# Kernel tuning notes

Hardware: AMD Instinct MI355X
Metric: run time of the kernel (lower is better)

The kernel has to match this reference:

```python
import jax, jax.numpy as jnp
import numpy as np

N, IN_DIM, D, H, M = 50000, 256, 256, 4, 3
C = D // H
E = 800000
EPS = 1e-5
NEG_SLOPE = 0.2


def setup_inputs() -> dict:
    key = jax.random.key(0)
    ks = jax.random.split(key, 16)
    inp = {
        'feat': jax.random.normal(ks[0], (N, IN_DIM), jnp.float32),
        'Wl': jax.random.normal(ks[1], (IN_DIM, D), jnp.float32) * (1.0 / np.sqrt(IN_DIM)),
        'bl': jnp.zeros((D,), jnp.float32),
        'Wr': jax.random.normal(ks[2], (IN_DIM, D), jnp.float32) * (1.0 / np.sqrt(IN_DIM)),
        'br': jnp.zeros((D,), jnp.float32),
        'attn_l': jax.random.normal(ks[3], (M, H, C), jnp.float32) * 0.1,
        'attn_r': jax.random.normal(ks[4], (M, H, C), jnp.float32) * 0.1,
        'rel_attn_l': jax.random.normal(ks[5], (H, C), jnp.float32) * 0.1,
        'rel_attn_r': jax.random.normal(ks[6], (H, C), jnp.float32) * 0.1,
        'ln_gamma': jnp.ones((D,), jnp.float32),
        'ln_beta': jnp.zeros((D,), jnp.float32),
    }
    for m in range(M):
        inp[f'src{m}'] = jax.random.randint(ks[7 + 2 * m], (E,), 0, N, jnp.int32)
        inp[f'dst{m}'] = jax.random.randint(ks[8 + 2 * m], (E,), 0, N, jnp.int32)
    return inp


def _latte_forward(feat, Wl, bl, Wr, br, attn_l, attn_r, rel_attn_l, rel_attn_r,
                   ln_gamma, ln_beta, edges):
    n = feat.shape[0]
    k = (feat @ Wl + bl).reshape(n, H, C)   # src projection
    v = (feat @ Wr + br).reshape(n, H, C)   # dst projection
    # per-node attention logit halves (equivalent to per-edge dot products)
    al = jnp.einsum('nhc,mhc->mnh', k, attn_l)  # [M,N,H]
    ar = jnp.einsum('nhc,mhc->mnh', v, attn_r)  # [M,N,H]
    hs = []
    for m, (src, dst) in enumerate(edges):
        att = al[m][src] + ar[m][dst]                  # [E,H]
        att = jax.nn.leaky_relu(att, NEG_SLOPE)        # attn_activation (dropout=identity, eval)
        # segment softmax over incoming edges of each dst node
        amax = jax.ops.segment_max(att, dst, num_segments=n)      # [N,H]
        ex = jnp.exp(att - amax[dst])                              # [E,H]
        denom = jax.ops.segment_sum(ex, dst, num_segments=n)      # [N,H]
        w = ex / denom[dst]                                        # softmax weights
        # message h = dst's v (faithful to edge_attention: {'h': edges.dst['v']})
        h = jax.ops.segment_sum(w[:, :, None] * v[dst], dst, num_segments=n)  # [N,H,C]
        hs.append(h)
    out = jnp.stack(hs + [v], axis=1)                  # [N,M+1,H,C]
    # relation-level beta attention; key = out[:, -1] = v
    alpha_l = jnp.einsum('nhc,hc->nh', v, rel_attn_l)          # [N,H]
    alpha_r = jnp.einsum('nrhc,hc->nrh', out, rel_attn_r)      # [N,M+1,H]
    beta = jax.nn.softmax(jax.nn.leaky_relu(alpha_l[:, None, :] + alpha_r, NEG_SLOPE), axis=2)
    o = (out * beta[..., None]).sum(axis=1).reshape(n, D)
    # LayerNorm
    mu = o.mean(axis=-1, keepdims=True)
    var = ((o - mu) ** 2).mean(axis=-1, keepdims=True)
    o = (o - mu) / jnp.sqrt(var + EPS) * ln_gamma + ln_beta
    return jax.nn.relu(o)  # dropout = identity in eval mode


def reference(feat, Wl, bl, Wr, br, attn_l, attn_r, rel_attn_l, rel_attn_r,
              ln_gamma, ln_beta, src0, dst0, src1, dst1, src2, dst2):
    edges = [(src0, dst0), (src1, dst1), (src2, dst2)]
    return _latte_forward(feat, Wl, bl, Wr, br, attn_l, attn_r,
                          rel_attn_l, rel_attn_r, ln_gamma, ln_beta, edges)
```

## Files before the change

kernel.cpp:

```cpp
#include <hip/hip_runtime.h>


#define NN 50000
#define NT 3125
#define NB 782
#define NEG 0.2f
#define EPSV 1e-5f

typedef __attribute__((ext_vector_type(8))) short bf16x8;
typedef __attribute__((ext_vector_type(4))) float f32x4;

#define LDS_FENCE() asm volatile("s_waitcnt lgkmcnt(0)" ::: "memory")

__device__ __forceinline__ short f2bf(float f) {
    unsigned u = __float_as_uint(f);
    u += 0x7fff + ((u >> 16) & 1);
    return (short)(u >> 16);
}

__device__ __forceinline__ void ld_g2l_16(void* lds, const void* g) {
    __builtin_amdgcn_global_load_lds(
        (const __attribute__((address_space(1))) unsigned int*)g,
        (__attribute__((address_space(3))) unsigned int*)lds, 16, 0, 0);
}
__device__ __forceinline__ void ld_g2l_4(void* lds, const void* g) {
    __builtin_amdgcn_global_load_lds(
        (const __attribute__((address_space(1))) unsigned int*)g,
        (__attribute__((address_space(3))) unsigned int*)lds, 4, 0, 0);
}

__global__ __launch_bounds__(256) void prep_kernel(
    const float* __restrict__ Wr, unsigned short* __restrict__ Wt)
{
    __shared__ float ws[32 * 256];
    int t = threadIdx.x;
    int kb = blockIdx.x * 32;
#pragma unroll
    for (int i = 0; i < 32; ++i)
        ws[i * 256 + t] = Wr[(size_t)(kb + i) * 256 + t];
    __syncthreads();
#pragma unroll
    for (int c = 0; c < 4; ++c) {
        bf16x8 o;
#pragma unroll
        for (int j = 0; j < 8; ++j)
            o[j] = f2bf(ws[(c * 8 + j) * 256 + t]);
        *reinterpret_cast<bf16x8*>(&Wt[(size_t)t * 256 + kb + c * 8]) = o;
    }
}

__global__ __launch_bounds__(256, 3) void fused_kernel(
    const float* __restrict__ feat, const unsigned short* __restrict__ Wt,
    const float* __restrict__ br, const float* __restrict__ rl,
    const float* __restrict__ rr, const float* __restrict__ gamma,
    const float* __restrict__ beta, float* __restrict__ out)
{
    __shared__ __align__(16) char smem[32768 + 4 * 4352];
    unsigned short* Bs = (unsigned short*)smem;
    const int t = threadIdx.x;
    const int wave = t >> 6, lane = t & 63;
    const int cl = lane & 15, quad = lane >> 4;
    const int tile = blockIdx.x * 4 + wave;
    const bool act = tile < NT;
    const int row0 = tile * 16;
    float* As = (float*)(smem + 32768 + wave * 4352);

    f32x4 acc[16];
#pragma unroll
    for (int i = 0; i < 16; ++i) acc[i] = (f32x4){0.f, 0.f, 0.f, 0.f};

#pragma unroll
    for (int chunk = 0; chunk < 4; ++chunk) {
        if (chunk) __syncthreads();
#pragma unroll
        for (int c = 0; c < 8; ++c) {
            int s = c * 256 + t;
            int n = s >> 3;
            int ksg = (s & 7) ^ (n & 7);
            ld_g2l_16(&Bs[(size_t)s * 8], Wt + n * 256 + chunk * 64 + ksg * 8);
        }
        if (act) {
#pragma unroll
            for (int i = 0; i < 16; ++i)
                ld_g2l_4(As + i * 68 + lane,
                         feat + (size_t)(row0 + i) * 256 + chunk * 64 + lane);
        }
        __syncthreads();
        if (act) {
#pragma unroll
            for (int kk = 0; kk < 2; ++kk) {
                int kb = kk * 32 + quad * 8;
                float4 a0 = *reinterpret_cast<const float4*>(As + cl * 68 + kb);
                float4 a1 = *reinterpret_cast<const float4*>(As + cl * 68 + kb + 4);
                bf16x8 af;
                af[0] = f2bf(a0.x); af[1] = f2bf(a0.y);
                af[2] = f2bf(a0.z); af[3] = f2bf(a0.w);
                af[4] = f2bf(a1.x); af[5] = f2bf(a1.y);
                af[6] = f2bf(a1.z); af[7] = f2bf(a1.w);
                int ks = kk * 4 + quad;
#pragma unroll
                for (int ct = 0; ct < 16; ++ct) {
                    int n = ct * 16 + cl;
                    bf16x8 bf = *reinterpret_cast<const bf16x8*>(
                        &Bs[(size_t)(n * 8 + (ks ^ (n & 7))) * 8]);
                    acc[ct] = __builtin_amdgcn_mfma_f32_16x16x32_bf16(af, bf, acc[ct], 0, 0, 0);
                }
            }
        }
    }
    __syncthreads();
    if (!act) return;

#pragma unroll
    for (int ct = 0; ct < 16; ++ct) {
        float bc = br[ct * 16 + cl];
#pragma unroll
        for (int r = 0; r < 4; ++r) acc[ct][r] += bc;
    }
    float z[4][4];
#pragma unroll
    for (int h = 0; h < 4; ++h) {
        float sl[4] = {0, 0, 0, 0}, sr[4] = {0, 0, 0, 0};
#pragma unroll
        for (int j = 0; j < 4; ++j) {
            int ct = h * 4 + j;
            float rlc = rl[ct * 16 + cl], rrc = rr[ct * 16 + cl];
#pragma unroll
            for (int r = 0; r < 4; ++r) {
                sl[r] += acc[ct][r] * rlc;
                sr[r] += acc[ct][r] * rrc;
            }
        }
#pragma unroll
        for (int off = 1; off < 16; off <<= 1)
#pragma unroll
            for (int r = 0; r < 4; ++r) {
                sl[r] += __shfl_xor(sl[r], off, 64);
                sr[r] += __shfl_xor(sr[r], off, 64);
            }
#pragma unroll
        for (int r = 0; r < 4; ++r) {
            float x = sl[r] + sr[r];
            z[h][r] = x > 0.f ? x : NEG * x;
        }
    }
    float gg[4][4];
#pragma unroll
    for (int r = 0; r < 4; ++r) {
        float mx = fmaxf(fmaxf(z[0][r], z[1][r]), fmaxf(z[2][r], z[3][r]));
        float e0 = __expf(z[0][r] - mx), e1 = __expf(z[1][r] - mx);
        float e2 = __expf(z[2][r] - mx), e3 = __expf(z[3][r] - mx);
        float inv = 1.f / (e0 + e1 + e2 + e3);
        gg[0][r] = e0 * inv; gg[1][r] = e1 * inv;
        gg[2][r] = e2 * inv; gg[3][r] = e3 * inv;
    }
    float s[4] = {0, 0, 0, 0}, s2[4] = {0, 0, 0, 0};
#pragma unroll
    for (int ct = 0; ct < 16; ++ct) {
        int h = ct >> 2;
#pragma unroll
        for (int r = 0; r < 4; ++r) {
            float o = acc[ct][r] * gg[h][r];
            acc[ct][r] = o;
            s[r] += o;
            s2[r] += o * o;
        }
    }
#pragma unroll
    for (int off = 1; off < 16; off <<= 1)
#pragma unroll
        for (int r = 0; r < 4; ++r) {
            s[r] += __shfl_xor(s[r], off, 64);
            s2[r] += __shfl_xor(s2[r], off, 64);
        }
    float mu[4], rstd[4];
#pragma unroll
    for (int r = 0; r < 4; ++r) {
        mu[r] = s[r] * (1.f / 256.f);
        float var = s2[r] * (1.f / 256.f) - mu[r] * mu[r];
        rstd[r] = rsqrtf(var + EPSV);
    }
    float* tb = reinterpret_cast<float*>(smem) + wave * 2048;
#pragma unroll
    for (int p = 0; p < 2; ++p) {
#pragma unroll
        for (int ct = 0; ct < 16; ++ct) {
            float ga = gamma[ct * 16 + cl], be = beta[ct * 16 + cl];
            float v0 = fmaxf((acc[ct][2 * p + 0] - mu[2 * p + 0]) * rstd[2 * p + 0] * ga + be, 0.f);
            float v1 = fmaxf((acc[ct][2 * p + 1] - mu[2 * p + 1]) * rstd[2 * p + 1] * ga + be, 0.f);
            tb[(quad * 2 + 0) * 256 + ct * 16 + cl] = v0;
            tb[(quad * 2 + 1) * 256 + ct * 16 + cl] = v1;
        }
        LDS_FENCE();
#pragma unroll
        for (int sl8 = 0; sl8 < 8; ++sl8) {
            int trow = (sl8 >> 1) * 4 + 2 * p + (sl8 & 1);
            float4 v4 = *reinterpret_cast<const float4*>(&tb[sl8 * 256 + lane * 4]);
            *reinterpret_cast<float4*>(&out[(size_t)(row0 + trow) * 256 + lane * 4]) = v4;
        }
        LDS_FENCE();
    }
}

extern "C" void kernel_launch(void* const* d_in, const int* in_sizes, int n_in,
                              void* d_out, int out_size, void* d_ws, size_t ws_size,
                              hipStream_t stream) {
    const float* feat = (const float*)d_in[0];
    const float* Wr   = (const float*)d_in[3];
    const float* br   = (const float*)d_in[4];
    const float* rl   = (const float*)d_in[7];
    const float* rr   = (const float*)d_in[8];
    const float* gam  = (const float*)d_in[9];
    const float* bet  = (const float*)d_in[10];
    float* out = (float*)d_out;
    unsigned short* Wt = (unsigned short*)d_ws;

    prep_kernel<<<8, 256, 0, stream>>>(Wr, Wt);
    fused_kernel<<<NB, 256, 0, stream>>>(feat, Wt, br, rl, rr, gam, bet, out);
}
```

Baseline: 190.3 us.

## Load A fragments directly to registers and use larger 512-thread blocks

A tiles are no longer staged through LDS. Each lane loads its feat row slice straight from global memory and converts it to bf16 once, before the K loop. Blocks grow to 8 waves sharing one 64KB B staging buffer loaded in two halves, so weight traffic per tile is amortized over more rows. Tiles are strided by grid size across waves. This cuts syncs and LDS traffic but raises register pressure (8 A fragments held) and limits residency to 2 blocks per CU.

```diff
diff --git a/kernel.cpp b/kernel.cpp
--- a/kernel.cpp
+++ b/kernel.cpp
@@ -3,7 +3,6 @@
 
 #define NN 50000
 #define NT 3125
-#define NB 782
 #define NEG 0.2f
 #define EPSV 1e-5f
 
@@ -22,11 +21,6 @@
     __builtin_amdgcn_global_load_lds(
         (const __attribute__((address_space(1))) unsigned int*)g,
         (__attribute__((address_space(3))) unsigned int*)lds, 16, 0, 0);
-}
-__device__ __forceinline__ void ld_g2l_4(void* lds, const void* g) {
-    __builtin_amdgcn_global_load_lds(
-        (const __attribute__((address_space(1))) unsigned int*)g,
-        (__attribute__((address_space(3))) unsigned int*)lds, 4, 0, 0);
 }
 
 __global__ __launch_bounds__(256) void prep_kernel(
@@ -49,60 +43,62 @@
     }
 }
 
-__global__ __launch_bounds__(256, 3) void fused_kernel(
+__global__ __launch_bounds__(512, 2) void fused_kernel(
     const float* __restrict__ feat, const unsigned short* __restrict__ Wt,
     const float* __restrict__ br, const float* __restrict__ rl,
     const float* __restrict__ rr, const float* __restrict__ gamma,
     const float* __restrict__ beta, float* __restrict__ out)
 {
-    __shared__ __align__(16) char smem[32768 + 4 * 4352];
+    __shared__ __align__(16) char smem[65536];
     unsigned short* Bs = (unsigned short*)smem;
     const int t = threadIdx.x;
     const int wave = t >> 6, lane = t & 63;
     const int cl = lane & 15, quad = lane >> 4;
-    const int tile = blockIdx.x * 4 + wave;
+    const int tile = blockIdx.x + 512 * wave;
     const bool act = tile < NT;
     const int row0 = tile * 16;
-    float* As = (float*)(smem + 32768 + wave * 4352);
 
     f32x4 acc[16];
 #pragma unroll
     for (int i = 0; i < 16; ++i) acc[i] = (f32x4){0.f, 0.f, 0.f, 0.f};
 
-#pragma unroll
-    for (int chunk = 0; chunk < 4; ++chunk) {
-        if (chunk) __syncthreads();
+    bf16x8 afr[8];
+    if (act) {
+        const float* arow = feat + (size_t)(row0 + cl) * 256;
+#pragma unroll
+        for (int kk8 = 0; kk8 < 8; ++kk8) {
+            int k0 = kk8 * 32 + quad * 8;
+            float4 a0 = *reinterpret_cast<const float4*>(arow + k0);
+            float4 a1 = *reinterpret_cast<const float4*>(arow + k0 + 4);
+            afr[kk8][0] = f2bf(a0.x); afr[kk8][1] = f2bf(a0.y);
+            afr[kk8][2] = f2bf(a0.z); afr[kk8][3] = f2bf(a0.w);
+            afr[kk8][4] = f2bf(a1.x); afr[kk8][5] = f2bf(a1.y);
+            afr[kk8][6] = f2bf(a1.z); afr[kk8][7] = f2bf(a1.w);
+        }
+    }
+
+#pragma unroll
+    for (int half = 0; half < 2; ++half) {
+        if (half) __syncthreads();
 #pragma unroll
         for (int c = 0; c < 8; ++c) {
-            int s = c * 256 + t;
-            int n = s >> 3;
-            int ksg = (s & 7) ^ (n & 7);
-            ld_g2l_16(&Bs[(size_t)s * 8], Wt + n * 256 + chunk * 64 + ksg * 8);
-        }
-        if (act) {
-#pragma unroll
-            for (int i = 0; i < 16; ++i)
-                ld_g2l_4(As + i * 68 + lane,
-                         feat + (size_t)(row0 + i) * 256 + chunk * 64 + lane);
+            int s = c * 512 + t;
+            int n = s >> 4;
+            int ks = (s & 15) ^ (n & 15);
+            const unsigned short* g = Wt + n * 256 + half * 128 + ks * 8;
+            ld_g2l_16(&Bs[(size_t)(c * 512 + wave * 64) * 8], g);
         }
         __syncthreads();
         if (act) {
 #pragma unroll
-            for (int kk = 0; kk < 2; ++kk) {
-                int kb = kk * 32 + quad * 8;
-                float4 a0 = *reinterpret_cast<const float4*>(As + cl * 68 + kb);
-                float4 a1 = *reinterpret_cast<const float4*>(As + cl * 68 + kb + 4);
-                bf16x8 af;
-                af[0] = f2bf(a0.x); af[1] = f2bf(a0.y);
-                af[2] = f2bf(a0.z); af[3] = f2bf(a0.w);
-                af[4] = f2bf(a1.x); af[5] = f2bf(a1.y);
-                af[6] = f2bf(a1.z); af[7] = f2bf(a1.w);
+            for (int kk = 0; kk < 4; ++kk) {
+                bf16x8 af = afr[half * 4 + kk];
                 int ks = kk * 4 + quad;
 #pragma unroll
                 for (int ct = 0; ct < 16; ++ct) {
                     int n = ct * 16 + cl;
                     bf16x8 bf = *reinterpret_cast<const bf16x8*>(
-                        &Bs[(size_t)(n * 8 + (ks ^ (n & 7))) * 8]);
+                        &Bs[(size_t)(n * 16 + (ks ^ (n & 15))) * 8]);
                     acc[ct] = __builtin_amdgcn_mfma_f32_16x16x32_bf16(af, bf, acc[ct], 0, 0, 0);
                 }
             }
@@ -216,5 +212,5 @@
     unsigned short* Wt = (unsigned short*)d_ws;
 
     prep_kernel<<<8, 256, 0, stream>>>(Wr, Wt);
-    fused_kernel<<<NB, 256, 0, stream>>>(feat, Wt, br, rl, rr, gam, bet, out);
-}
+    fused_kernel<<<512, 512, 0, stream>>>(feat, Wt, br, rl, rr, gam, bet, out);
+}
```

Measured after the change: 155.5 us. 1.22x faster.
